# Kernel tuning notes

Hardware: AMD Instinct MI355X
Metric: run time of the kernel (lower is better)

## Reference

```python
import jax, jax.numpy as jnp
import numpy as np

B, N, G, C = 4, 4000, 64, 91
H, W = 800.0, 1333.0
FG_THRESH, BG_THRESH = 0.5, 0.5
SCORE_THRESH, NMS_THRESH = 0.05, 0.5
DET_PER_IMG = 100
PRE_NMS_TOPK = 2048   # candidates entering NMS per image
MIN_SIZE = 0.01
BBOX_XFORM_CLIP = float(np.log(1000.0 / 16.0))
WX, WY, WW, WH = 10.0, 10.0, 5.0, 5.0  # bbox_reg_weights


def _rand_boxes(key, shape):
    k1, k2 = jax.random.split(key)
    xy = jax.random.uniform(k1, shape[:-1] + (2,)) * jnp.array([W * 0.8, H * 0.8], jnp.float32)
    wh = jax.random.uniform(k2, shape[:-1] + (2,)) * jnp.array([W * 0.2, H * 0.2], jnp.float32) + 2.0
    return jnp.concatenate([xy, xy + wh], axis=-1)


def setup_inputs():
    key = jax.random.key(0)
    ks = jax.random.split(key, 5)
    proposals = _rand_boxes(ks[0], (B, N, 4))
    gt_boxes = _rand_boxes(ks[1], (B, G, 4))
    gt_labels = jax.random.randint(ks[2], (B, G), 1, C)
    class_logits = jax.random.normal(ks[3], (B, N, C), dtype=jnp.float32)
    box_regression = jax.random.normal(ks[4], (B, N, C * 4), dtype=jnp.float32) * 0.1
    return {"proposals": proposals, "gt_boxes": gt_boxes, "gt_labels": gt_labels,
            "class_logits": class_logits, "box_regression": box_regression}


def box_iou(a, b):
    # a [A,4], b [B,4] -> [A,B]
    area_a = (a[:, 2] - a[:, 0]) * (a[:, 3] - a[:, 1])
    area_b = (b[:, 2] - b[:, 0]) * (b[:, 3] - b[:, 1])
    lt = jnp.maximum(a[:, None, :2], b[None, :, :2])
    rb = jnp.minimum(a[:, None, 2:], b[None, :, 2:])
    wh = jnp.clip(rb - lt, 0.0)
    inter = wh[..., 0] * wh[..., 1]
    return inter / (area_a[:, None] + area_b[None, :] - inter)


def encode(gt, prop):
    # BoxCoder.encode with weights (10,10,5,5)
    pw = prop[:, 2] - prop[:, 0]; ph = prop[:, 3] - prop[:, 1]
    px = prop[:, 0] + 0.5 * pw;  py = prop[:, 1] + 0.5 * ph
    gw = gt[:, 2] - gt[:, 0];    gh = gt[:, 3] - gt[:, 1]
    gx = gt[:, 0] + 0.5 * gw;    gy = gt[:, 1] + 0.5 * gh
    return jnp.stack([WX * (gx - px) / pw, WY * (gy - py) / ph,
                      WW * jnp.log(gw / pw), WH * jnp.log(gh / ph)], axis=1)


def decode(deltas, boxes):
    # deltas [N,C,4], boxes [N,4] -> [N,C,4]
    pw = boxes[:, 2] - boxes[:, 0]; ph = boxes[:, 3] - boxes[:, 1]
    px = boxes[:, 0] + 0.5 * pw;    py = boxes[:, 1] + 0.5 * ph
    dx = deltas[..., 0] / WX; dy = deltas[..., 1] / WY
    dw = jnp.minimum(deltas[..., 2] / WW, BBOX_XFORM_CLIP)
    dh = jnp.minimum(deltas[..., 3] / WH, BBOX_XFORM_CLIP)
    cx = dx * pw[:, None] + px[:, None]; cy = dy * ph[:, None] + py[:, None]
    w = jnp.exp(dw) * pw[:, None];       h = jnp.exp(dh) * ph[:, None]
    return jnp.stack([cx - 0.5 * w, cy - 0.5 * h, cx + 0.5 * w, cy + 0.5 * h], axis=-1)


def _image_fwd(prop, gt_b, gt_l, logits, regr):
    # --- assign_targets_to_proposals (with add_gt_proposals) ---
    props_all = jnp.concatenate([prop, gt_b], axis=0)          # [N+G,4]
    iou = box_iou(gt_b, props_all)                             # [G,N+G]
    matched_vals = iou.max(axis=0)
    matches = iou.argmax(axis=0)
    lbl = jnp.where(matched_vals >= FG_THRESH, gt_l[matches],
                    jnp.where(matched_vals < BG_THRESH, 0, -1))
    reg_targets = encode(gt_b[matches], props_all)             # [N+G,4]

    # --- postprocess_detections: decode + softmax + per-class NMS ---
    deltas = regr.reshape(N, C, 4)
    pb = decode(deltas, prop)                                  # [N,C,4]
    pb = jnp.stack([jnp.clip(pb[..., 0], 0.0, W), jnp.clip(pb[..., 1], 0.0, H),
                    jnp.clip(pb[..., 2], 0.0, W), jnp.clip(pb[..., 3], 0.0, H)], axis=-1)
    scores = jax.nn.softmax(logits, axis=-1)                   # [N,C]
    boxes_f = pb[:, 1:].reshape(-1, 4)                         # drop background class
    scores_f = scores[:, 1:].reshape(-1)
    labels_f = jnp.broadcast_to(jnp.arange(1, C), (N, C - 1)).reshape(-1)
    wf = boxes_f[:, 2] - boxes_f[:, 0]; hf = boxes_f[:, 3] - boxes_f[:, 1]
    valid = (scores_f > SCORE_THRESH) & (wf >= MIN_SIZE) & (hf >= MIN_SIZE)
    masked = jnp.where(valid, scores_f, -1.0)
    top_vals, top_idx = jax.lax.top_k(masked, PRE_NMS_TOPK)    # score-sorted candidates
    cb = boxes_f[top_idx]; cl = labels_f[top_idx]; cs = scores_f[top_idx]
    cv = top_vals > 0.0
    # batched_nms via per-class coordinate offset
    off = cl.astype(cb.dtype) * (max(W, H) + 1.0)
    ob = cb + off[:, None]
    iou_c = box_iou(ob, ob)                                    # [M,M]
    order = jnp.arange(PRE_NMS_TOPK)

    def body(i, keep):
        sup = keep[i] & (iou_c[i] > NMS_THRESH) & (order > i)
        return keep & ~sup

    keep = jax.lax.fori_loop(0, PRE_NMS_TOPK, body, cv)
    rank = jnp.cumsum(keep) - 1
    out_pos = jnp.where(keep & (rank < DET_PER_IMG), rank, DET_PER_IMG)  # OOB -> drop
    det_b = jnp.zeros((DET_PER_IMG, 4), cb.dtype).at[out_pos].set(cb, mode='drop')
    det_s = jnp.zeros((DET_PER_IMG,), cs.dtype).at[out_pos].set(cs, mode='drop')
    det_l = jnp.zeros((DET_PER_IMG,), cl.dtype).at[out_pos].set(cl, mode='drop')
    det = jnp.concatenate([det_b, det_s[:, None]], axis=-1)    # [K,5]
    return det, reg_targets, lbl, det_l


def reference(proposals, gt_boxes, gt_labels, class_logits, box_regression):
    return jax.vmap(_image_fwd)(proposals, gt_boxes, gt_labels, class_logits, box_regression)
```

## Files before the change

kernel.cpp:

```cpp
#include <hip/hip_runtime.h>
#include <cstdint>
#include <cstddef>

#define Bn   4
#define Nn   4000
#define Gn   64
#define Cn   91
#define FGC  90
#define RPW  4
#define BLKROWS 16
#define NBLKI 250
#define CAPSEG 128
#define SLOTSI (NBLKI*CAPSEG)
#define SELD 12288
#define RBLK2 32
#define STCAP 4096
#define MSEL 2048
#define DETK 100

__device__ __constant__ float kW = 1333.0f;
__device__ __constant__ float kH = 800.0f;
#define XCLIP 4.135166556742356f
#define OFFMUL 1334.0f

#define NB 9216
#define SBIAS 0x3D400000u

typedef __attribute__((ext_vector_type(2))) unsigned long long u64x2;

#define OUT_DET  0
#define OUT_REG  (Bn*DETK*5)
#define OUT_LBL  (OUT_REG + Bn*(Nn+Gn)*4)
#define OUT_DETL (OUT_LBL + Bn*(Nn+Gn))

__device__ __forceinline__ void decode_box(float4 p, float4 d,
                                           float& bx1, float& by1, float& bx2, float& by2) {
    float pw = p.z - p.x, ph = p.w - p.y;
    float px = p.x + 0.5f * pw, py = p.y + 0.5f * ph;
    float dx = d.x / 10.0f, dy = d.y / 10.0f;
    float dw = fminf(d.z / 5.0f, XCLIP), dh = fminf(d.w / 5.0f, XCLIP);
    float cx = dx * pw + px, cy = dy * ph + py;
    float w = expf(dw) * pw, h = expf(dh) * ph;
    bx1 = fminf(fmaxf(cx - 0.5f * w, 0.0f), kW);
    by1 = fminf(fmaxf(cy - 0.5f * h, 0.0f), kH);
    bx2 = fminf(fmaxf(cx + 0.5f * w, 0.0f), kW);
    by2 = fminf(fmaxf(cy + 0.5f * h, 0.0f), kH);
}

__device__ __forceinline__ unsigned score_bucket(unsigned sb) {
    unsigned h = (sb - SBIAS) >> 12;
    return h > (NB - 1) ? (NB - 1) : h;
}

__global__ __launch_bounds__(256) void cand_assign_k(const float* __restrict__ logits,
                                                     const float* __restrict__ props,
                                                     const float* __restrict__ gtb,
                                                     const int* __restrict__ gtl,
                                                     float* __restrict__ out,
                                                     unsigned long long* __restrict__ keys,
                                                     unsigned int* __restrict__ cnt) {
    int wave = threadIdx.x >> 6, lane = threadIdx.x & 63;
    if (blockIdx.x >= Bn * NBLKI) {
        __shared__ float4 sg[Gn];
        int ablk = blockIdx.x - Bn * NBLKI;
        int b = ablk >> 4;
        int p = (ablk & 15) * 256 + threadIdx.x;
        if (threadIdx.x < Gn) sg[threadIdx.x] = ((const float4*)(gtb + (size_t)b * Gn * 4))[threadIdx.x];
        __syncthreads();
        if (p >= Nn + Gn) return;
        float4 pb = (p < Nn) ? ((const float4*)(props + (size_t)b * Nn * 4))[p] : sg[p - Nn];
        float areap = (pb.z - pb.x) * (pb.w - pb.y);
        float best = -1.0f; int bi = 0;
        #pragma unroll 4
        for (int g = 0; g < Gn; ++g) {
            float4 gb = sg[g];
            float xx1 = fmaxf(gb.x, pb.x), yy1 = fmaxf(gb.y, pb.y);
            float xx2 = fminf(gb.z, pb.z), yy2 = fminf(gb.w, pb.w);
            float iw = fmaxf(xx2 - xx1, 0.0f), ih = fmaxf(yy2 - yy1, 0.0f);
            float inter = iw * ih;
            float areag = (gb.z - gb.x) * (gb.w - gb.y);
            float iou = inter / (areag + areap - inter);
            if (iou > best) { best = iou; bi = g; }
        }
        float4 gb = sg[bi];
        float pw = pb.z - pb.x, ph = pb.w - pb.y;
        float px = pb.x + 0.5f * pw, py = pb.y + 0.5f * ph;
        float gw = gb.z - gb.x, gh = gb.w - gb.y;
        float gx = gb.x + 0.5f * gw, gy = gb.y + 0.5f * gh;
        float* rr = out + OUT_REG + ((size_t)b * (Nn + Gn) + p) * 4;
        rr[0] = 10.0f * (gx - px) / pw;
        rr[1] = 10.0f * (gy - py) / ph;
        rr[2] = 5.0f * logf(gw / pw);
        rr[3] = 5.0f * logf(gh / ph);
        out[OUT_LBL + (size_t)b * (Nn + Gn) + p] = (best >= 0.5f) ? (float)gtl[b * Gn + bi] : 0.0f;
        return;
    }
    __shared__ unsigned lcnt;
    int blk = blockIdx.x;
    if (threadIdx.x == 0) lcnt = 0;
    int rowbase = blk * BLKROWS + wave * RPW;
    int b = blk / NBLKI;
    int nbase = rowbase - b * Nn;
    bool has1 = (lane + 64) < Cn;
    const float* z = logits + (size_t)rowbase * Cn;
    float v0[RPW], v1[RPW], m[RPW], e[RPW], t0[RPW], t1[RPW];
    #pragma unroll
    for (int r = 0; r < RPW; ++r) {
        v0[r] = z[r * Cn + lane];
        v1[r] = has1 ? z[r * Cn + lane + 64] : -INFINITY;
        m[r] = fmaxf(v0[r], v1[r]);
    }
    #pragma unroll
    for (int o = 32; o; o >>= 1) {
        #pragma unroll
        for (int r = 0; r < RPW; ++r) m[r] = fmaxf(m[r], __shfl_xor(m[r], o));
    }
    #pragma unroll
    for (int r = 0; r < RPW; ++r) {
        t0[r] = expf(v0[r] - m[r]);
        t1[r] = has1 ? expf(v1[r] - m[r]) : 0.0f;
        e[r] = t0[r] + t1[r];
    }
    #pragma unroll
    for (int o = 32; o; o >>= 1) {
        #pragma unroll
        for (int r = 0; r < RPW; ++r) e[r] += __shfl_xor(e[r], o);
    }
    unsigned long long keyA[RPW], keyB[RPW];
    bool vA[RPW], vB[RPW];
    #pragma unroll
    for (int r = 0; r < RPW; ++r) {
        float s0 = t0[r] / e[r];
        float s1 = has1 ? (t1[r] / e[r]) : 0.0f;
        vA[r] = (lane >= 1) && (s0 > 0.05f);
        vB[r] = has1 && (s1 > 0.05f);
        unsigned idxA = (unsigned)((nbase + r) * FGC + lane - 1);
        unsigned idxB = (unsigned)((nbase + r) * FGC + lane + 63);
        keyA[r] = ((unsigned long long)__float_as_uint(s0) << 32) | (unsigned long long)(~idxA);
        keyB[r] = ((unsigned long long)__float_as_uint(s1) << 32) | (unsigned long long)(~idxB);
    }
    __syncthreads();
    unsigned long long mk[2 * RPW];
    #pragma unroll
    for (int r = 0; r < RPW; ++r) { mk[2*r] = __ballot(vA[r]); mk[2*r+1] = __ballot(vB[r]); }
    unsigned tot = 0, pre[2 * RPW];
    #pragma unroll
    for (int q = 0; q < 2 * RPW; ++q) { pre[q] = tot; tot += (unsigned)__popcll(mk[q]); }
    if (tot) {
        unsigned base = 0;
        if (lane == 0) base = atomicAdd(&lcnt, tot);
        base = __shfl(base, 0);
        unsigned long long lmask = (lane == 63) ? (~0ull >> 1) : ((1ull << lane) - 1);
        size_t segbase = (size_t)blk * CAPSEG;
        #pragma unroll
        for (int r = 0; r < RPW; ++r) {
            if (vA[r]) {
                unsigned pos = base + pre[2*r] + (unsigned)__popcll(mk[2*r] & lmask);
                if (pos < CAPSEG) keys[segbase + pos] = keyA[r];
            }
            if (vB[r]) {
                unsigned pos = base + pre[2*r+1] + (unsigned)__popcll(mk[2*r+1] & lmask);
                if (pos < CAPSEG) keys[segbase + pos] = keyB[r];
            }
        }
    }
    __syncthreads();
    if (threadIdx.x == 0) cnt[blk] = lcnt;
}

__global__ __launch_bounds__(128) void compact_dense_k(const unsigned long long* __restrict__ keys,
                                                       const unsigned int* __restrict__ cnt,
                                                       unsigned long long* __restrict__ sel) {
    __shared__ unsigned sc[NBLKI];
    int g = blockIdx.x;
    int b = g / NBLKI, segloc = g - b * NBLKI;
    int tid = threadIdx.x;
    for (int s = tid; s < NBLKI; s += 128) {
        unsigned c = cnt[b * NBLKI + s];
        sc[s] = c > CAPSEG ? CAPSEG : c;
    }
    __syncthreads();
    unsigned off = 0;
    for (int s = 0; s < segloc; ++s) off += sc[s];
    unsigned count = sc[segloc];
    if ((unsigned)tid < count) {
        unsigned dst = off + (unsigned)tid;
        if (dst < SELD)
            sel[(size_t)b * SELD + dst] = keys[(size_t)g * CAPSEG + tid];
    }
}

__global__ __launch_bounds__(256) void pivot_rank_k(const unsigned long long* __restrict__ sel,
                                                    const unsigned int* __restrict__ cnt,
                                                    const float* __restrict__ props,
                                                    const float* __restrict__ regr,
                                                    float* __restrict__ cb, float* __restrict__ ob,
                                                    float* __restrict__ sc, int* __restrict__ lab) {
    int b = blockIdx.x >> 5, k = blockIdx.x & (RBLK2 - 1);
    int tid = threadIdx.x, lane = tid & 63, wv = tid >> 6;
    __shared__ unsigned hist[NB];
    __shared__ __align__(16) unsigned long long staged[STCAP + 8];
    __shared__ unsigned wtot[4];
    __shared__ unsigned sV, sT, lsel;
    if (wv == 0) {
        unsigned vsum = 0;
        #pragma unroll
        for (int q = 0; q < 4; ++q) {
            int s = lane + q * 64;
            if (s < NBLKI) { unsigned c = cnt[b * NBLKI + s]; vsum += c > CAPSEG ? CAPSEG : c; }
        }
        #pragma unroll
        for (int o = 32; o; o >>= 1) vsum += __shfl_xor(vsum, o);
        if (lane == 0) sV = vsum;
    }
    for (int h = tid; h < NB; h += 256) hist[h] = 0;
    if (tid == 0) { sT = NB; lsel = 0; }
    __syncthreads();
    unsigned V = sV; if (V > SELD) V = SELD;
    if (V == 0) return;
    const unsigned long long* selb = sel + (size_t)b * SELD;
    const uint2* selb2 = (const uint2*)selb;
    for (unsigned i = (unsigned)tid; i < V; i += 256)
        atomicAdd(&hist[score_bucket(selb2[i].y)], 1u);
    __syncthreads();
    unsigned hc[36]; unsigned ssum = 0;
    #pragma unroll
    for (int q = 0; q < 36; ++q) { hc[q] = hist[tid * 36 + q]; ssum += hc[q]; }
    unsigned x = ssum;
    #pragma unroll
    for (int o = 1; o < 64; o <<= 1) { unsigned v = __shfl_down(x, o); if (lane + o < 64) x += v; }
    if (lane == 0) wtot[wv] = x;
    __syncthreads();
    unsigned above = 0, total = 0;
    #pragma unroll
    for (int i2 = 0; i2 < 4; ++i2) { unsigned w2 = wtot[i2]; total += w2; if (i2 > wv) above += w2; }
    unsigned K2 = total < MSEL ? total : MSEL;
    {
        unsigned run = (x - ssum) + above;
        #pragma unroll
        for (int q = 35; q >= 0; --q) {
            unsigned c = hc[q], lo = run;
            run += c;
            if (lo < K2 && K2 <= run) sT = (unsigned)(tid * 36 + q);
        }
    }
    __syncthreads();
    unsigned T = sT;
    unsigned long long lmask = (lane == 63) ? (~0ull >> 1) : ((1ull << lane) - 1);
    for (unsigned i = (unsigned)tid; i < V; i += 256) {
        unsigned long long key = selb[i];
        bool selv = score_bucket((unsigned)(key >> 32)) >= T;
        unsigned long long mb = __ballot(selv);
        unsigned cw = (unsigned)__popcll(mb);
        if (cw) {
            unsigned basew = 0;
            if (lane == 0) basew = atomicAdd(&lsel, cw);
            basew = __shfl(basew, 0);
            if (selv) {
                unsigned pos = basew + (unsigned)__popcll(mb & lmask);
                if (pos < STCAP) staged[pos] = key;
            }
        }
    }
    __syncthreads();
    unsigned n2 = lsel; if (n2 > STCAP) n2 = STCAP;
    if (tid < 8) staged[n2 + tid] = 0ull;
    __syncthreads();
    unsigned sub = (unsigned)(k * 256 + tid);
    bool act = sub < V;
    unsigned long long mk = act ? selb[sub] : 0ull;
    if (act) act = score_bucket((unsigned)(mk >> 32)) >= T;
    if (!__any(act)) return;
    unsigned npair = ((n2 + 7) & ~7u) >> 1;
    const u64x2* sk2 = (const u64x2*)staged;
    unsigned cntg = 0;
    for (unsigned j = 0; j < npair; j += 4) {
        u64x2 a = sk2[j], b2 = sk2[j + 1], c2 = sk2[j + 2], d2 = sk2[j + 3];
        cntg += (unsigned)(a.x > mk) + (unsigned)(a.y > mk)
              + (unsigned)(b2.x > mk) + (unsigned)(b2.y > mk)
              + (unsigned)(c2.x > mk) + (unsigned)(c2.y > mk)
              + (unsigned)(d2.x > mk) + (unsigned)(d2.y > mk);
    }
    if (act && cntg < MSEL) {
        int t = b * MSEL + (int)cntg;
        unsigned idx = ~(unsigned)mk;
        int n = idx / FGC, cm1 = idx - n * FGC;
        int c = cm1 + 1;
        float score = __uint_as_float((unsigned)(mk >> 32));
        int row = b * Nn + n;
        float4 p = ((const float4*)props)[row];
        float4 d = ((const float4*)regr)[(size_t)row * Cn + c];
        float bx1, by1, bx2, by2;
        decode_box(p, d, bx1, by1, bx2, by2);
        float off = (float)c * OFFMUL;
        cb[t * 4 + 0] = bx1; cb[t * 4 + 1] = by1; cb[t * 4 + 2] = bx2; cb[t * 4 + 3] = by2;
        ob[t * 4 + 0] = bx1 + off; ob[t * 4 + 1] = by1 + off;
        ob[t * 4 + 2] = bx2 + off; ob[t * 4 + 3] = by2 + off;
        sc[t] = score; lab[t] = c;
    }
}

__global__ __launch_bounds__(256) void nmsmat_k(const float* __restrict__ ob,
                                                unsigned long long* __restrict__ M) {
    int blk = blockIdx.x;
    int b = blk >> 8, rc = (blk >> 5) & 7, w = blk & 31;
    int i = rc * 256 + threadIdx.x;
    size_t mi = ((size_t)b * MSEL + i) * 32 + w;
    if (w * 64 + 63 <= rc * 256) {
        M[mi] = 0ull;
        return;
    }
    __shared__ float4 sj[64];
    const float4* obf4 = (const float4*)(ob + (size_t)b * MSEL * 4);
    if (threadIdx.x < 64) sj[threadIdx.x] = obf4[w * 64 + threadIdx.x];
    __syncthreads();
    float4 bi = obf4[i];
    float areai = (bi.z - bi.x) * (bi.w - bi.y);
    unsigned long long bits = 0ull;
    #pragma unroll 16
    for (int tt = 0; tt < 64; ++tt) {
        int j = w * 64 + tt;
        float4 bj = sj[tt];
        float xx1 = fmaxf(bi.x, bj.x), yy1 = fmaxf(bi.y, bj.y);
        float xx2 = fminf(bi.z, bj.z), yy2 = fminf(bi.w, bj.w);
        float iw = fmaxf(xx2 - xx1, 0.0f), ih = fmaxf(yy2 - yy1, 0.0f);
        float inter = iw * ih;
        float areaj = (bj.z - bj.x) * (bj.w - bj.y);
        float iou = inter / (areai + areaj - inter);
        if ((iou > 0.5f) && (j > i)) bits |= (1ull << tt);
    }
    M[mi] = bits;
}

__global__ __launch_bounds__(64) void scan_k(const unsigned long long* __restrict__ M,
                                             const unsigned int* __restrict__ cnt,
                                             const float* __restrict__ cb,
                                             const float* __restrict__ sc,
                                             const int* __restrict__ lab,
                                             float* __restrict__ out) {
    int b = blockIdx.x, lane = threadIdx.x;
    const bool ld = lane < 32;
    unsigned vsum = 0;
    #pragma unroll
    for (int q = 0; q < 4; ++q) {
        int s = lane + q * 64;
        if (s < NBLKI) { unsigned c = cnt[b * NBLKI + s]; vsum += c > CAPSEG ? CAPSEG : c; }
    }
    #pragma unroll
    for (int o = 32; o; o >>= 1) vsum += __shfl_xor(vsum, o);
    int validN = (int)(vsum < MSEL ? vsum : MSEL);
    unsigned long long keep = 0ull;
    if (ld) {
        int base = lane * 64;
        keep = (base + 64 <= validN) ? ~0ull
             : (base >= validN ? 0ull : ((1ull << (validN - base)) - 1ull));
    }
    unsigned kLo = (unsigned)keep, kHi = (unsigned)(keep >> 32);
    __shared__ int keptIdx[DETK];
    const unsigned long long* Mb = M + (size_t)b * MSEL * 32;
    int kcount = 0;
    unsigned long long Abuf[16], Bbuf[16];
    #pragma unroll
    for (int k = 0; k < 16; ++k) Abuf[k] = ld ? Mb[(size_t)k * 32 + lane] : 0ull;
    for (int g = 0; g < 128; g += 2) {
        #pragma unroll
        for (int k = 0; k < 16; ++k)
            Bbuf[k] = ld ? Mb[(size_t)((g + 1) * 16 + k) * 32 + lane] : 0ull;
        {
            int base = g * 16;
            int rl = base >> 6, sh = base & 31;
            unsigned half = (base >> 5) & 1;
            #pragma unroll
            for (int k = 0; k < 16; ++k) {
                unsigned kw = half ? kHi : kLo;
                unsigned bitv = (__builtin_amdgcn_readlane(kw, rl) >> (sh + k)) & 1u;
                if (bitv) {
                    unsigned long long m = Abuf[k];
                    kLo &= ~(unsigned)m; kHi &= ~(unsigned)(m >> 32);
                    if (kcount < DETK && lane == 0) keptIdx[kcount] = base + k;
                    ++kcount;
                }
            }
        }
        if (kcount >= DETK) break;
        if (g + 2 < 128) {
            #pragma unroll
            for (int k = 0; k < 16; ++k)
                Abuf[k] = ld ? Mb[(size_t)((g + 2) * 16 + k) * 32 + lane] : 0ull;
        }
        {
            int base = (g + 1) * 16;
            int rl = base >> 6, sh = base & 31;
            unsigned half = (base >> 5) & 1;
            #pragma unroll
            for (int k = 0; k < 16; ++k) {
                unsigned kw = half ? kHi : kLo;
                unsigned bitv = (__builtin_amdgcn_readlane(kw, rl) >> (sh + k)) & 1u;
                if (bitv) {
                    unsigned long long m = Bbuf[k];
                    kLo &= ~(unsigned)m; kHi &= ~(unsigned)(m >> 32);
                    if (kcount < DETK && lane == 0) keptIdx[kcount] = base + k;
                    ++kcount;
                }
            }
        }
        if (kcount >= DETK) break;
    }
    __syncthreads();
    int kept100 = kcount < DETK ? kcount : DETK;
    for (int r = lane; r < kept100; r += 64) {
        int i = keptIdx[r];
        int slot = b * MSEL + i;
        float* dr = out + OUT_DET + ((size_t)b * DETK + r) * 5;
        dr[0] = cb[slot * 4 + 0]; dr[1] = cb[slot * 4 + 1];
        dr[2] = cb[slot * 4 + 2]; dr[3] = cb[slot * 4 + 3];
        dr[4] = sc[slot];
        out[OUT_DETL + b * DETK + r] = (float)lab[slot];
    }
    for (int r = kept100 + lane; r < DETK; r += 64) {
        float* dr = out + OUT_DET + ((size_t)b * DETK + r) * 5;
        dr[0] = dr[1] = dr[2] = dr[3] = dr[4] = 0.0f;
        out[OUT_DETL + b * DETK + r] = 0.0f;
    }
}

extern "C" void kernel_launch(void* const* d_in, const int* in_sizes, int n_in,
                              void* d_out, int out_size, void* d_ws, size_t ws_size,
                              hipStream_t stream) {
    const float* props  = (const float*)d_in[0];
    const float* gtb    = (const float*)d_in[1];
    const int*   gtl    = (const int*)d_in[2];
    const float* logits = (const float*)d_in[3];
    const float* regr   = (const float*)d_in[4];
    float* out = (float*)d_out;

    char* w = (char*)d_ws;
    unsigned int* cnt           = (unsigned int*)(w + 0);
    unsigned long long* keys    = (unsigned long long*)(w + 4096);
    unsigned long long* sel     = (unsigned long long*)(w + 1028096);
    float* cb                   = (float*)(w + 1421312);
    float* ob                   = (float*)(w + 1552384);
    float* sc                   = (float*)(w + 1683456);
    int* lab                    = (int*)(w + 1716224);
    unsigned long long* M       = (unsigned long long*)(w + 1748992);
    (void)ws_size; (void)in_sizes; (void)n_in; (void)out_size;

    cand_assign_k<<<Bn * NBLKI + 64, 256, 0, stream>>>(logits, props, gtb, gtl, out, keys, cnt);
    compact_dense_k<<<Bn * NBLKI, 128, 0, stream>>>(keys, cnt, sel);
    pivot_rank_k<<<Bn * RBLK2, 256, 0, stream>>>(sel, cnt, props, regr, cb, ob, sc, lab);
    nmsmat_k<<<Bn * 256, 256, 0, stream>>>(ob, M);
    scan_k<<<Bn, 64, 0, stream>>>(M, cnt, cb, sc, lab, out);
}
```

Measured before the change: 87.95 us.

## Build score histogram in compaction kernel via global atomics instead of per-block LDS

Moves the score-bucket histogram out of pivot_rank_k, where every block rebuilt it in shared memory from all selected keys, into compact_dense_k. There it is accumulated with global atomics as keys are written, and a set of extra blocks in cand_assign_k zeroes it beforehand. The rank kernel now just reads the precomputed histogram with vector loads, which also frees a large LDS allocation and should raise occupancy. It also grows the per-image rank block count to 36 so all candidates are covered, and unrolls the comparison loop wider. The cost is contention on the global atomics and a changed workspace layout.

```diff
diff --git a/kernel.cpp b/kernel.cpp
--- a/kernel.cpp
+++ b/kernel.cpp
@@ -13,7 +13,7 @@
 #define CAPSEG 128
 #define SLOTSI (NBLKI*CAPSEG)
 #define SELD 12288
-#define RBLK2 32
+#define RBLK2 36
 #define STCAP 4096
 #define MSEL 2048
 #define DETK 100
@@ -25,6 +25,7 @@
 
 #define NB 9216
 #define SBIAS 0x3D400000u
+#define ZHIST_BLKS 36
 
 typedef __attribute__((ext_vector_type(2))) unsigned long long u64x2;
 
@@ -58,8 +59,14 @@
                                                      const int* __restrict__ gtl,
                                                      float* __restrict__ out,
                                                      unsigned long long* __restrict__ keys,
-                                                     unsigned int* __restrict__ cnt) {
+                                                     unsigned int* __restrict__ cnt,
+                                                     uint4* __restrict__ histz) {
     int wave = threadIdx.x >> 6, lane = threadIdx.x & 63;
+    if (blockIdx.x >= Bn * NBLKI + 64) {
+        int i = (blockIdx.x - (Bn * NBLKI + 64)) * 256 + threadIdx.x;
+        if (i < NB * Bn / 4) histz[i] = make_uint4(0, 0, 0, 0);
+        return;
+    }
     if (blockIdx.x >= Bn * NBLKI) {
         __shared__ float4 sg[Gn];
         int ablk = blockIdx.x - Bn * NBLKI;
@@ -170,7 +177,8 @@
 
 __global__ __launch_bounds__(128) void compact_dense_k(const unsigned long long* __restrict__ keys,
                                                        const unsigned int* __restrict__ cnt,
-                                                       unsigned long long* __restrict__ sel) {
+                                                       unsigned long long* __restrict__ sel,
+                                                       unsigned int* __restrict__ hist) {
     __shared__ unsigned sc[NBLKI];
     int g = blockIdx.x;
     int b = g / NBLKI, segloc = g - b * NBLKI;
@@ -185,21 +193,24 @@
     unsigned count = sc[segloc];
     if ((unsigned)tid < count) {
         unsigned dst = off + (unsigned)tid;
-        if (dst < SELD)
-            sel[(size_t)b * SELD + dst] = keys[(size_t)g * CAPSEG + tid];
-    }
-}
-
-__global__ __launch_bounds__(256) void pivot_rank_k(const unsigned long long* __restrict__ sel,
-                                                    const unsigned int* __restrict__ cnt,
-                                                    const float* __restrict__ props,
-                                                    const float* __restrict__ regr,
-                                                    float* __restrict__ cb, float* __restrict__ ob,
-                                                    float* __restrict__ sc, int* __restrict__ lab) {
-    int b = blockIdx.x >> 5, k = blockIdx.x & (RBLK2 - 1);
+        if (dst < SELD) {
+            unsigned long long key = keys[(size_t)g * CAPSEG + tid];
+            sel[(size_t)b * SELD + dst] = key;
+            atomicAdd(&hist[b * NB + score_bucket((unsigned)(key >> 32))], 1u);
+        }
+    }
+}
+
+__global__ __launch_bounds__(256) void pivot_rank2_k(const unsigned long long* __restrict__ sel,
+                                                     const unsigned int* __restrict__ cnt,
+                                                     const unsigned int* __restrict__ hist,
+                                                     const float* __restrict__ props,
+                                                     const float* __restrict__ regr,
+                                                     float* __restrict__ cb, float* __restrict__ ob,
+                                                     float* __restrict__ sc, int* __restrict__ lab) {
+    int b = blockIdx.x / RBLK2, k = blockIdx.x % RBLK2;
     int tid = threadIdx.x, lane = tid & 63, wv = tid >> 6;
-    __shared__ unsigned hist[NB];
-    __shared__ __align__(16) unsigned long long staged[STCAP + 8];
+    __shared__ __align__(16) unsigned long long staged[STCAP + 16];
     __shared__ unsigned wtot[4];
     __shared__ unsigned sV, sT, lsel;
     if (wv == 0) {
@@ -213,19 +224,18 @@
         for (int o = 32; o; o >>= 1) vsum += __shfl_xor(vsum, o);
         if (lane == 0) sV = vsum;
     }
-    for (int h = tid; h < NB; h += 256) hist[h] = 0;
     if (tid == 0) { sT = NB; lsel = 0; }
     __syncthreads();
     unsigned V = sV; if (V > SELD) V = SELD;
     if (V == 0) return;
-    const unsigned long long* selb = sel + (size_t)b * SELD;
-    const uint2* selb2 = (const uint2*)selb;
-    for (unsigned i = (unsigned)tid; i < V; i += 256)
-        atomicAdd(&hist[score_bucket(selb2[i].y)], 1u);
-    __syncthreads();
+    const uint4* h4 = (const uint4*)(hist + b * NB);
     unsigned hc[36]; unsigned ssum = 0;
     #pragma unroll
-    for (int q = 0; q < 36; ++q) { hc[q] = hist[tid * 36 + q]; ssum += hc[q]; }
+    for (int q = 0; q < 9; ++q) {
+        uint4 t4 = h4[tid * 9 + q];
+        hc[q*4+0] = t4.x; hc[q*4+1] = t4.y; hc[q*4+2] = t4.z; hc[q*4+3] = t4.w;
+        ssum += t4.x + t4.y + t4.z + t4.w;
+    }
     unsigned x = ssum;
     #pragma unroll
     for (int o = 1; o < 64; o <<= 1) { unsigned v = __shfl_down(x, o); if (lane + o < 64) x += v; }
@@ -247,6 +257,7 @@
     __syncthreads();
     unsigned T = sT;
     unsigned long long lmask = (lane == 63) ? (~0ull >> 1) : ((1ull << lane) - 1);
+    const unsigned long long* selb = sel + (size_t)b * SELD;
     for (unsigned i = (unsigned)tid; i < V; i += 256) {
         unsigned long long key = selb[i];
         bool selv = score_bucket((unsigned)(key >> 32)) >= T;
@@ -264,22 +275,27 @@
     }
     __syncthreads();
     unsigned n2 = lsel; if (n2 > STCAP) n2 = STCAP;
-    if (tid < 8) staged[n2 + tid] = 0ull;
+    if (tid < 16) staged[n2 + tid] = 0ull;
     __syncthreads();
     unsigned sub = (unsigned)(k * 256 + tid);
     bool act = sub < V;
     unsigned long long mk = act ? selb[sub] : 0ull;
     if (act) act = score_bucket((unsigned)(mk >> 32)) >= T;
     if (!__any(act)) return;
-    unsigned npair = ((n2 + 7) & ~7u) >> 1;
+    unsigned npair = ((n2 + 15) & ~15u) >> 1;
     const u64x2* sk2 = (const u64x2*)staged;
     unsigned cntg = 0;
-    for (unsigned j = 0; j < npair; j += 4) {
-        u64x2 a = sk2[j], b2 = sk2[j + 1], c2 = sk2[j + 2], d2 = sk2[j + 3];
+    for (unsigned j = 0; j < npair; j += 8) {
+        u64x2 a = sk2[j],     b2 = sk2[j + 1], c2 = sk2[j + 2], d2 = sk2[j + 3];
+        u64x2 e2 = sk2[j + 4], f2 = sk2[j + 5], g2 = sk2[j + 6], h2 = sk2[j + 7];
         cntg += (unsigned)(a.x > mk) + (unsigned)(a.y > mk)
               + (unsigned)(b2.x > mk) + (unsigned)(b2.y > mk)
               + (unsigned)(c2.x > mk) + (unsigned)(c2.y > mk)
-              + (unsigned)(d2.x > mk) + (unsigned)(d2.y > mk);
+              + (unsigned)(d2.x > mk) + (unsigned)(d2.y > mk)
+              + (unsigned)(e2.x > mk) + (unsigned)(e2.y > mk)
+              + (unsigned)(f2.x > mk) + (unsigned)(f2.y > mk)
+              + (unsigned)(g2.x > mk) + (unsigned)(g2.y > mk)
+              + (unsigned)(h2.x > mk) + (unsigned)(h2.y > mk);
     }
     if (act && cntg < MSEL) {
         int t = b * MSEL + (int)cntg;
@@ -436,18 +452,20 @@
 
     char* w = (char*)d_ws;
     unsigned int* cnt           = (unsigned int*)(w + 0);
-    unsigned long long* keys    = (unsigned long long*)(w + 4096);
-    unsigned long long* sel     = (unsigned long long*)(w + 1028096);
-    float* cb                   = (float*)(w + 1421312);
-    float* ob                   = (float*)(w + 1552384);
-    float* sc                   = (float*)(w + 1683456);
-    int* lab                    = (int*)(w + 1716224);
-    unsigned long long* M       = (unsigned long long*)(w + 1748992);
+    unsigned int* hist          = (unsigned int*)(w + 4096);
+    unsigned long long* keys    = (unsigned long long*)(w + 151552);
+    unsigned long long* sel     = (unsigned long long*)(w + 1175552);
+    float* cb                   = (float*)(w + 1568768);
+    float* ob                   = (float*)(w + 1699840);
+    float* sc                   = (float*)(w + 1830912);
+    int* lab                    = (int*)(w + 1863680);
+    unsigned long long* M       = (unsigned long long*)(w + 1896448);
     (void)ws_size; (void)in_sizes; (void)n_in; (void)out_size;
 
-    cand_assign_k<<<Bn * NBLKI + 64, 256, 0, stream>>>(logits, props, gtb, gtl, out, keys, cnt);
-    compact_dense_k<<<Bn * NBLKI, 128, 0, stream>>>(keys, cnt, sel);
-    pivot_rank_k<<<Bn * RBLK2, 256, 0, stream>>>(sel, cnt, props, regr, cb, ob, sc, lab);
+    cand_assign_k<<<Bn * NBLKI + 64 + ZHIST_BLKS, 256, 0, stream>>>(logits, props, gtb, gtl, out,
+                                                                    keys, cnt, (uint4*)hist);
+    compact_dense_k<<<Bn * NBLKI, 128, 0, stream>>>(keys, cnt, sel, hist);
+    pivot_rank2_k<<<Bn * RBLK2, 256, 0, stream>>>(sel, cnt, hist, props, regr, cb, ob, sc, lab);
     nmsmat_k<<<Bn * 256, 256, 0, stream>>>(ob, M);
     scan_k<<<Bn, 64, 0, stream>>>(M, cnt, cb, sc, lab, out);
 }
```

After: 85.90 us. 2.3% less time.
